# Performance work log

Hardware: AMD Instinct MI355X
Metric: run time of the kernel (lower is better)

## Reference

```python
import jax, jax.numpy as jnp
import numpy as np

DIM = 384
HEADS = 8


def setup_inputs() -> dict:
    key = jax.random.key(0)
    ks = jax.random.split(key, 8)
    d = DIM
    return {
        "x": jax.random.normal(ks[0], (4, d, 128, 128), jnp.float32),
        "message": jax.random.normal(ks[1], (4, d, 128, 128), jnp.float32),
        "temperature": jnp.ones((HEADS, 1, 1), jnp.float32),
        "qkv_w": jax.random.normal(ks[2], (3 * d, d), jnp.float32) * 0.02,   # 1x1 conv weight
        "dw_w": jax.random.normal(ks[3], (3 * d, 1, 3, 3), jnp.float32) * 0.02,  # depthwise 3x3
        "proj_w": jax.random.normal(ks[4], (d, d), jnp.float32) * 0.02,     # project_out 1x1
        "lin_w": jax.random.normal(ks[5], (d, 2 * d), jnp.float32) * 0.02,  # nn.Linear weight [out,in]
        "lin_b": jnp.zeros((d,), jnp.float32),
    }


def _qkv_branch(t, qkv_w, dw_w):
    # 1x1 conv (pointwise) then depthwise 3x3, groups = 3*dim
    y = jnp.einsum('oc,bchw->bohw', qkv_w, t)
    y = jax.lax.conv_general_dilated(
        y, dw_w, window_strides=(1, 1), padding='SAME',
        dimension_numbers=('NCHW', 'OIHW', 'NCHW'),
        feature_group_count=dw_w.shape[0])
    return jnp.split(y, 3, axis=1)  # q, k, v each [b, dim, h, w]


def _to_heads(t):
    b, c, h, w = t.shape
    return t.reshape(b, HEADS, c // HEADS, h * w)  # [b, head, c, n]


def _l2norm(t):
    # torch F.normalize(dim=-1, eps=1e-12)
    n = jnp.sqrt(jnp.sum(t * t, axis=-1, keepdims=True))
    return t / jnp.maximum(n, 1e-12)


def reference(x, message, temperature, qkv_w, dw_w, proj_w, lin_w, lin_b):
    b, c, h, w = x.shape
    q, k, v = (_to_heads(t) for t in _qkv_branch(x, qkv_w, dw_w))
    q_m, k_m, v_m = (_to_heads(t) for t in _qkv_branch(message, qkv_w, dw_w))

    k_c = jnp.concatenate([k, k_m], axis=2)   # [b, head, 2c, n]
    v_c = jnp.concatenate([v, v_m], axis=2)

    q = _l2norm(q)
    k_c = _l2norm(k_c)
    q_m = _l2norm(q_m)

    # channel attention: [b, head, c, 2c]
    attn1 = jax.nn.softmax(jnp.einsum('bhcn,bhdn->bhcd', q, k_c) * temperature, axis=-1)
    attn2 = jax.nn.softmax(jnp.einsum('bhcn,bhdn->bhcd', q_m, k_c) * temperature, axis=-1)

    out1 = jnp.einsum('bhcd,bhdn->bhcn', attn1, v_c)  # [b, head, c, n]
    out2 = jnp.einsum('bhcd,bhdn->bhcn', attn2, v_c)

    # 'b head c (h w) -> b (h w) (head c)'
    out1 = out1.transpose(0, 3, 1, 2).reshape(b, h * w, c)
    out2 = out2.transpose(0, 3, 1, 2).reshape(b, h * w, c)

    cat = jnp.concatenate([out1, out2], axis=2)  # [b, n, 2c]
    out = cat @ lin_w.T + lin_b                  # [b, n, c]

    # 'b (h w) c -> b c h w'
    out = out.transpose(0, 2, 1).reshape(b, c, h, w)
    out = jnp.einsum('oc,bchw->bohw', proj_w, out)
    return out
```

## Files before the change

kernel.cpp:

```cpp
#include <hip/hip_runtime.h>

typedef unsigned short u16;
typedef unsigned int u32;

#define BATCH 4
#define CDIM 384
#define IMG 128
#define HW 16384
#define QKVC 1152
#define NHEADS 8
#define CHD 48
#define DD2 96
#define KFIN 768

typedef __attribute__((ext_vector_type(8))) short bf16x8;
typedef __attribute__((ext_vector_type(4))) float f32x4;

__device__ __forceinline__ u16 f2bf(float f){
  union { float f; u32 u; } v; v.f = f;
  u32 u = v.u;
  u32 r = (u + 0x7fffu + ((u >> 16) & 1u)) >> 16;
  return (u16)r;
}
__device__ __forceinline__ float bf2f(u16 h){
  union { u32 u; float f; } v; v.u = ((u32)h) << 16;
  return v.f;
}

#define OFF_QKVX  ((size_t)0)
#define OFF_QKVM  ((size_t)150994944)
#define OFF_T     ((size_t)301989888)
#define OFF_SSQ   ((size_t)339738624)
#define OFF_S     ((size_t)339775488)
#define OFF_ATTN  ((size_t)340955136)
#define OFF_AFINB ((size_t)342134784)
#define OFF_W2    ((size_t)344494080)
#define OFF_B2    ((size_t)345673728)
#define OFF_WB    ((size_t)345675264)

typedef __attribute__((address_space(1))) const u32 gas_u32;
typedef __attribute__((address_space(3))) u32 las_u32;
__device__ __forceinline__ void gl_lds16(const u16* g, u16* l){
  __builtin_amdgcn_global_load_lds((gas_u32*)g, (las_u32*)l, 16, 0, 0);
}

__device__ __forceinline__ u16* t_row(u16* T0, u16* qkvm, int par, int ch){
  if (par == 0) return T0 + (size_t)ch * HW;
  int bq = ch / 384;
  int rr = ch - bq * 384;
  return qkvm + ((size_t)bq * QKVC + 2 * CDIM + rr) * HW;
}

__global__ void __launch_bounds__(256) k_w2(const float* __restrict__ proj,
                                            const float* __restrict__ lin,
                                            const float* __restrict__ linb,
                                            const float* __restrict__ qkvw,
                                            float* __restrict__ W2,
                                            float* __restrict__ b2,
                                            u16* __restrict__ Wb){
  int idx = blockIdx.x * 256 + threadIdx.x;
  if (idx < CDIM * KFIN){
    int o = idx / KFIN, d = idx % KFIN;
    float acc = 0.f;
    for (int c = 0; c < CDIM; c++)
      acc = fmaf(proj[o * CDIM + c], lin[c * KFIN + d], acc);
    W2[idx] = acc;
  }
  if (idx < CDIM){
    float acc = 0.f;
    for (int c = 0; c < CDIM; c++)
      acc = fmaf(proj[idx * CDIM + c], linb[c], acc);
    b2[idx] = acc;
  }
  if (idx < QKVC * CDIM) Wb[idx] = f2bf(qkvw[idx]);
}

__device__ __forceinline__ void loadrow(const u16* __restrict__ src, int r, int cg, float* o){
  if ((unsigned)r >= IMG){
    #pragma unroll
    for (int i = 0; i < 18; i++) o[i] = 0.f;
    return;
  }
  const u16* p = src + (size_t)r * IMG + cg * 16;
  uint4 v0 = *(const uint4*)p;
  uint4 v1 = *(const uint4*)(p + 8);
  u32 ww[8] = {v0.x, v0.y, v0.z, v0.w, v1.x, v1.y, v1.z, v1.w};
  #pragma unroll
  for (int i = 0; i < 8; i++){
    union { u32 u; float f; } lo, hi;
    lo.u = ww[i] << 16;
    hi.u = ww[i] & 0xffff0000u;
    o[1 + 2 * i] = lo.f;
    o[2 + 2 * i] = hi.f;
  }
  o[0]  = (cg > 0) ? bf2f(p[-1]) : 0.f;
  o[17] = (cg < 7) ? bf2f(p[16]) : 0.f;
}

__global__ void __launch_bounds__(256) k_stage(
    int t, int npw, int ndw,
    const u16* __restrict__ Wb, u16* __restrict__ Bt,
    u16* __restrict__ T0, u16* __restrict__ qkvx, u16* __restrict__ qkvm,
    const float* __restrict__ x, const float* __restrict__ msg,
    const float* __restrict__ dww, float* __restrict__ ssq){
  __shared__ __align__(16) u16 smem[16384];
  int bid = blockIdx.x;
  int tid = threadIdx.x;

  if (bid < npw){
    int z = t - 1, par = z & 1;
    const u16* B = Bt + (size_t)z * HW * CDIM;
    u16* As = smem;
    u16* Bs = smem + 8192;
    int swz = (bid & 7) * 144 + (bid >> 3);
    int bx = swz % 9, by = swz / 9;
    int m0 = bx * 128, n0 = by * 128;
    int w = tid >> 6, lane = tid & 63;
    int wy = w >> 1, wx = w & 1;
    int lm = lane & 15, q = lane >> 4;

    int srow = w * 16 + (lane >> 2);
    int scol = (lane & 3) * 8;
    const u16* ga = Wb + (size_t)(m0 + srow) * CDIM + scol;
    const u16* gb = B + (size_t)(n0 + srow) * CDIM + scol;
    u16* la = As + srow * 32 + scol;
    u16* lb = Bs + srow * 32 + scol;

    f32x4 acc[4][4];
    #pragma unroll
    for (int i = 0; i < 4; i++)
      #pragma unroll
      for (int j = 0; j < 4; j++) acc[i][j] = (f32x4){0.f,0.f,0.f,0.f};

#define PW_STAGE(buf, k0) do{ \
      gl_lds16(ga + (k0),             la + (buf) * 4096); \
      gl_lds16(ga + 64*CDIM + (k0),   la + (buf) * 4096 + 2048); \
      gl_lds16(gb + (k0),             lb + (buf) * 4096); \
      gl_lds16(gb + 64*CDIM + (k0),   lb + (buf) * 4096 + 2048); \
    }while(0)

    PW_STAGE(0, 0);
    __syncthreads();
    int cur = 0;
    for (int kt = 0; kt < 12; kt++){
      if (kt < 11) PW_STAGE(cur ^ 1, (kt + 1) * 32);
      bf16x8 af[4], bfr[4];
      #pragma unroll
      for (int i = 0; i < 4; i++)
        af[i] = *(const bf16x8*)&As[cur * 4096 + (wy * 64 + i * 16 + lm) * 32 + q * 8];
      #pragma unroll
      for (int j = 0; j < 4; j++)
        bfr[j] = *(const bf16x8*)&Bs[cur * 4096 + (wx * 64 + j * 16 + lm) * 32 + q * 8];
      #pragma unroll
      for (int i = 0; i < 4; i++)
        #pragma unroll
        for (int j = 0; j < 4; j++)
          acc[i][j] = __builtin_amdgcn_mfma_f32_16x16x32_bf16(af[i], bfr[j], acc[i][j], 0, 0, 0);
      __syncthreads();
      cur ^= 1;
    }
#undef PW_STAGE
    #pragma unroll
    for (int i = 0; i < 4; i++){
      #pragma unroll
      for (int r = 0; r < 4; r++){
        int row = m0 + wy * 64 + i * 16 + q * 4 + r;
        u16* cp = t_row(T0, qkvm, par, row) + n0 + wx * 64 + lm;
        #pragma unroll
        for (int j = 0; j < 4; j++)
          cp[j * 16] = f2bf(acc[i][j][r]);
      }
    }

  } else if (bid < npw + ndw){
    int ch = bid - npw;
    int z = t - 2, par = z & 1;
    const u16* src = t_row(T0, qkvm, par, ch);
    u16* dst;
    if (ch < 2 * CDIM){
      u16* qd = ((z >> 2) ? qkvm : qkvx) + (size_t)(z & 3) * QKVC * HW;
      dst = qd + (size_t)ch * HW;
    } else {
      dst = Bt + (size_t)z * HW * CDIM + (size_t)(ch - 2 * CDIM) * HW;
    }
    float w[9];
    #pragma unroll
    for (int t9 = 0; t9 < 9; t9++) w[t9] = dww[ch * 9 + t9];
    int rg = tid >> 3, cg = tid & 7;
    int r0 = rg * 4;
    float ra[18], rb[18], rc[18];
    loadrow(src, r0 - 1, cg, ra);
    loadrow(src, r0,     cg, rb);
    float ss = 0.f;
    #pragma unroll
    for (int rr = 0; rr < 4; rr++){
      int r = r0 + rr;
      loadrow(src, r + 1, cg, rc);
      u32 pk[8];
      #pragma unroll
      for (int xx = 0; xx < 16; xx++){
        float a2 = w[0] * ra[xx];
        a2 = fmaf(w[1], ra[xx + 1], a2);
        a2 = fmaf(w[2], ra[xx + 2], a2);
        a2 = fmaf(w[3], rb[xx],     a2);
        a2 = fmaf(w[4], rb[xx + 1], a2);
        a2 = fmaf(w[5], rb[xx + 2], a2);
        a2 = fmaf(w[6], rc[xx],     a2);
        a2 = fmaf(w[7], rc[xx + 1], a2);
        a2 = fmaf(w[8], rc[xx + 2], a2);
        ss = fmaf(a2, a2, ss);
        u16 hv = f2bf(a2);
        if (xx & 1) pk[xx >> 1] |= (u32)hv << 16;
        else        pk[xx >> 1]  = (u32)hv;
      }
      *(uint4*)(dst + (size_t)r * IMG + cg * 16)     = *(uint4*)&pk[0];
      *(uint4*)(dst + (size_t)r * IMG + cg * 16 + 8) = *(uint4*)&pk[4];
      #pragma unroll
      for (int ii = 0; ii < 18; ii++){ ra[ii] = rb[ii]; rb[ii] = rc[ii]; }
    }
    if (ch < 2 * CDIM){
      float* red = (float*)smem;
      red[tid] = ss;
      __syncthreads();
      for (int s = 128; s > 0; s >>= 1){
        if (tid < s) red[tid] += red[tid + s];
        __syncthreads();
      }
      if (tid == 0) ssq[(size_t)z * QKVC + ch] = red[0];
    }

  } else {
    int cb = bid - npw - ndw;
    int z = t;
    const float* src = (z < 4 ? x : msg) + (size_t)(z & 3) * CDIM * HW;
    u16* dstz = Bt + (size_t)z * HW * CDIM;
    int n0 = (cb & 127) * 128;
    int c0 = (cb >> 7) * 64;
    u16 (*tile)[130] = (u16(*)[130])smem;
    #pragma unroll
    for (int i = 0; i < 8; i++){
      int c = (tid >> 5) + i * 8;
      int nq = tid & 31;
      float4 v = *(const float4*)(src + (size_t)(c0 + c) * HW + n0 + nq * 4);
      u32 p0 = (u32)f2bf(v.x) | ((u32)f2bf(v.y) << 16);
      u32 p1 = (u32)f2bf(v.z) | ((u32)f2bf(v.w) << 16);
      *(u32*)&tile[c][nq * 4]     = p0;
      *(u32*)&tile[c][nq * 4 + 2] = p1;
    }
    __syncthreads();
    #pragma unroll
    for (int u = 0; u < 2; u++){
      int idx = tid + u * 256;
      int n = idx >> 2, j = idx & 3;
      u32 pk[8];
      #pragma unroll
      for (int p = 0; p < 8; p++)
        pk[p] = (u32)tile[j * 16 + 2 * p][n] | ((u32)tile[j * 16 + 2 * p + 1][n] << 16);
      u16* dp = dstz + (size_t)(n0 + n) * CDIM + c0 + j * 16;
      *(uint4*)dp       = *(uint4*)&pk[0];
      *(uint4*)(dp + 8) = *(uint4*)&pk[4];
    }
  }
}

#define LCHUNK 1024
__global__ void __launch_bounds__(256) k_tail(u16* __restrict__ qkvx,
                                              u16* __restrict__ qkvm,
                                              float* __restrict__ S,
                                              const u16* __restrict__ Bt){
  __shared__ u16 tile[48][136];
  int bid = blockIdx.x;
  int tid = threadIdx.x;

  if (bid < 512){
    int nc = bid & 15;
    int bh = bid >> 4;
    int b = bh & 3, h = bh >> 2;
    int w = tid >> 6, lane = tid & 63;
    int wy = w >> 1, wx = w & 1;
    int lm = lane & 15, quad = lane >> 4;

    const u16* ap[3]; const u16* bp[3];
    #pragma unroll
    for (int i = 0; i < 3; i++){
      int g = wy * 48 + i * 16 + lm;
      int c = (g < 48) ? g : g - 48;
      ap[i] = ((g < 48) ? qkvx : qkvm) + ((size_t)b * QKVC + h * CHD + c) * HW;
      int d = wx * 48 + i * 16 + lm;
      int cc = (d < 48) ? d : d - 48;
      bp[i] = ((d < 48) ? qkvx : qkvm) + ((size_t)b * QKVC + CDIM + h * CHD + cc) * HW;
    }
    f32x4 acc[3][3];
    #pragma unroll
    for (int i = 0; i < 3; i++)
      #pragma unroll
      for (int j = 0; j < 3; j++) acc[i][j] = (f32x4){0.f,0.f,0.f,0.f};

    int nbeg = nc * LCHUNK + quad * 8;
    int nend = nc * LCHUNK + LCHUNK;
    for (int n = nbeg; n < nend; n += 32){
      bf16x8 af[3], bfr[3];
      #pragma unroll
      for (int i = 0; i < 3; i++) af[i]  = *(const bf16x8*)(ap[i] + n);
      #pragma unroll
      for (int j = 0; j < 3; j++) bfr[j] = *(const bf16x8*)(bp[j] + n);
      #pragma unroll
      for (int i = 0; i < 3; i++)
        #pragma unroll
        for (int j = 0; j < 3; j++)
          acc[i][j] = __builtin_amdgcn_mfma_f32_16x16x32_bf16(af[i], bfr[j], acc[i][j], 0, 0, 0);
    }
    #pragma unroll
    for (int i = 0; i < 3; i++){
      #pragma unroll
      for (int r = 0; r < 4; r++){
        int g = wy * 48 + i * 16 + quad * 4 + r;
        int iq = (g >= 48) ? 1 : 0;
        int c = iq ? g - 48 : g;
        float* Sp = S + (((size_t)(iq * BATCH + b) * NHEADS + h) * CHD + c) * DD2;
        #pragma unroll
        for (int j = 0; j < 3; j++)
          atomicAdd(&Sp[wx * 48 + j * 16 + lm], acc[i][j][r]);
      }
    }
  } else {
    int v = bid - 512;
    int nb = v & 127;
    int h = (v >> 7) & 7;
    int z = v >> 10;
    int inp = z >> 2, b = z & 3;
    const u16* vcn = Bt + (size_t)z * HW * CDIM;
    int n0 = nb * 128;
    u16* vt = (h < 4 ? qkvx : qkvm) + ((size_t)b * QKVC + 2 * CDIM) * HW;
    int dbase = (h & 3) * 96 + inp * 48;
    #pragma unroll
    for (int j = 0; j < 3; j++){
      int i = tid + j * 256;
      int row = i >> 4, c8 = i & 15;
      uint4 vv = *(const uint4*)(vcn + (size_t)(h * 48 + row) * HW + n0 + c8 * 8);
      *(uint4*)&tile[row][c8 * 8] = vv;
    }
    __syncthreads();
    int n = tid >> 1, half = tid & 1;
    u16* dstp = vt + (size_t)(n0 + n) * CDIM + dbase + half * 24;
    #pragma unroll
    for (int u = 0; u < 3; u++){
      u32 pk[4];
      #pragma unroll
      for (int p = 0; p < 4; p++){
        int c = half * 24 + u * 8 + p * 2;
        pk[p] = (u32)tile[c][n] | ((u32)tile[c + 1][n] << 16);
      }
      *(uint4*)(dstp + u * 8) = *(uint4*)pk;
    }
  }
}

__global__ void __launch_bounds__(128) k_softmax(const float* __restrict__ S,
                                                 const float* __restrict__ ssq,
                                                 const float* __restrict__ temp,
                                                 float* __restrict__ attn){
  int row = blockIdx.x;
  int c = row % CHD;
  int h = (row / CHD) % NHEADS;
  int b = (row / (CHD * NHEADS)) % BATCH;
  int iq = row / (CHD * NHEADS * BATCH);
  int tid = threadIdx.x;
  __shared__ float sh[128];
  const float* Sp = S + (size_t)row * DD2;
  float ssq_q = ssq[(iq * BATCH + b) * QKVC + h * CHD + c];
  float nq = fmaxf(sqrtf(ssq_q), 1e-12f);
  float tmp = temp[h];
  float logit = -1e30f;
  int d = tid;
  if (d < DD2){
    float ssq_k = ssq[((d < CHD ? 0 : 1) * BATCH + b) * QKVC + CDIM + h * CHD + (d % CHD)];
    float nk = fmaxf(sqrtf(ssq_k), 1e-12f);
    logit = Sp[d] * tmp / (nq * nk);
  }
  sh[tid] = logit; __syncthreads();
  for (int s = 64; s > 0; s >>= 1){
    if (tid < s) sh[tid] = fmaxf(sh[tid], sh[tid + s]);
    __syncthreads();
  }
  float mx = sh[0]; __syncthreads();
  float e = (d < DD2) ? expf(logit - mx) : 0.f;
  sh[tid] = e; __syncthreads();
  for (int s = 64; s > 0; s >>= 1){
    if (tid < s) sh[tid] += sh[tid + s];
    __syncthreads();
  }
  float sum = sh[0];
  if (d < DD2) attn[(size_t)row * DD2 + d] = e / sum;
}

__global__ void __launch_bounds__(128) k_mmat(const float* __restrict__ attn,
                                              const float* __restrict__ W2,
                                              u16* __restrict__ AfinB){
  int oz = blockIdx.x;
  int h = blockIdx.y;
  int b = blockIdx.z;
  __shared__ float a1[CHD * DD2];
  __shared__ float a2[CHD * DD2];
  int tid = threadIdx.x;
  const float* A1 = attn + ((size_t)(0 * BATCH + b) * NHEADS + h) * CHD * DD2;
  const float* A2 = attn + ((size_t)(1 * BATCH + b) * NHEADS + h) * CHD * DD2;
  for (int i = tid; i < CHD * DD2; i += 128){ a1[i] = A1[i]; a2[i] = A2[i]; }
  __syncthreads();
  int e = tid;
  if (e < DD2){
    for (int oo = 0; oo < 8; oo++){
      int o = oz * 8 + oo;
      float acc = 0.f;
      #pragma unroll 4
      for (int cc = 0; cc < CHD; cc++){
        acc = fmaf(W2[o * KFIN + h * CHD + cc],        a1[cc * DD2 + e], acc);
        acc = fmaf(W2[o * KFIN + CDIM + h * CHD + cc], a2[cc * DD2 + e], acc);
      }
      AfinB[((size_t)b * CDIM + o) * KFIN + h * DD2 + e] = f2bf(acc);
    }
  }
}

__global__ void __launch_bounds__(256) k_fin(const u16* __restrict__ AfB,
                                             const u16* __restrict__ qkvx,
                                             const u16* __restrict__ qkvm,
                                             const float* __restrict__ b2,
                                             float* __restrict__ out){
  __shared__ __align__(16) u16 As[2 * 4096];
  __shared__ __align__(16) u16 Bs[2 * 4096];
  int orig = blockIdx.x;
  int swz = (orig & 7) * 192 + (orig >> 3);
  int m = swz % 3;
  int rest = swz / 3;
  int n0 = (rest & 127) * 128;
  int bz = rest >> 7;
  int m0 = m * 128;
  int tid = threadIdx.x;
  int w = tid >> 6, lane = tid & 63;
  int wy = w >> 1, wx = w & 1;
  int lm = lane & 15, q = lane >> 4;

  int srow = w * 16 + (lane >> 2);
  int scol = (lane & 3) * 8;
  const u16* A = AfB + (size_t)bz * CDIM * KFIN;
  const u16* ga  = A + (size_t)(m0 + srow) * KFIN + scol;
  const u16* gb0 = qkvx + ((size_t)bz * QKVC + 2 * CDIM) * HW + (size_t)(n0 + srow) * CDIM + scol;
  const u16* gb1 = qkvm + ((size_t)bz * QKVC + 2 * CDIM) * HW + (size_t)(n0 + srow) * CDIM + scol;
  u16* la = As + srow * 32 + scol;
  u16* lb = Bs + srow * 32 + scol;

  f32x4 acc[4][4];
  #pragma unroll
  for (int i = 0; i < 4; i++)
    #pragma unroll
    for (int j = 0; j < 4; j++) acc[i][j] = (f32x4){0.f,0.f,0.f,0.f};

#define FIN_STAGE(buf, t) do{ \
    int hp_ = (t) >= 12; \
    int k0_ = ((t) - hp_ * 12) * 32; \
    const u16* gb_ = hp_ ? gb1 : gb0; \
    gl_lds16(ga + hp_ * CDIM + k0_,            la + (buf) * 4096); \
    gl_lds16(ga + hp_ * CDIM + k0_ + 64*KFIN,  la + (buf) * 4096 + 2048); \
    gl_lds16(gb_ + k0_,                        lb + (buf) * 4096); \
    gl_lds16(gb_ + k0_ + 64*CDIM,              lb + (buf) * 4096 + 2048); \
  }while(0)

  FIN_STAGE(0, 0);
  __syncthreads();
  int cur = 0;
  for (int t = 0; t < 24; t++){
    if (t < 23) FIN_STAGE(cur ^ 1, t + 1);
    bf16x8 af[4], bfr[4];
    #pragma unroll
    for (int i = 0; i < 4; i++)
      af[i] = *(const bf16x8*)&As[cur * 4096 + (wy * 64 + i * 16 + lm) * 32 + q * 8];
    #pragma unroll
    for (int j = 0; j < 4; j++)
      bfr[j] = *(const bf16x8*)&Bs[cur * 4096 + (wx * 64 + j * 16 + lm) * 32 + q * 8];
    #pragma unroll
    for (int i = 0; i < 4; i++)
      #pragma unroll
      for (int j = 0; j < 4; j++)
        acc[i][j] = __builtin_amdgcn_mfma_f32_16x16x32_bf16(af[i], bfr[j], acc[i][j], 0, 0, 0);
    __syncthreads();
    cur ^= 1;
  }
#undef FIN_STAGE
  #pragma unroll
  for (int i = 0; i < 4; i++){
    #pragma unroll
    for (int r = 0; r < 4; r++){
      int row = m0 + wy * 64 + i * 16 + q * 4 + r;
      float bv = b2[row];
      float* cp = out + (size_t)bz * CDIM * HW + (size_t)row * HW + n0 + wx * 64 + lm;
      #pragma unroll
      for (int j = 0; j < 4; j++)
        cp[j * 16] = acc[i][j][r] + bv;
    }
  }
}

extern "C" void kernel_launch(void* const* d_in, const int* in_sizes, int n_in,
                              void* d_out, int out_size, void* d_ws, size_t ws_size,
                              hipStream_t stream){
  const float* x      = (const float*)d_in[0];
  const float* msg    = (const float*)d_in[1];
  const float* temp   = (const float*)d_in[2];
  const float* qkv_w  = (const float*)d_in[3];
  const float* dw_w   = (const float*)d_in[4];
  const float* proj_w = (const float*)d_in[5];
  const float* lin_w  = (const float*)d_in[6];
  const float* lin_b  = (const float*)d_in[7];
  float* out = (float*)d_out;

  char* ws = (char*)d_ws;
  u16*   qkvx  = (u16*)(ws + OFF_QKVX);
  u16*   qkvm  = (u16*)(ws + OFF_QKVM);
  u16*   T0    = (u16*)(ws + OFF_T);
  float* ssq   = (float*)(ws + OFF_SSQ);
  float* S     = (float*)(ws + OFF_S);
  float* attn  = (float*)(ws + OFF_ATTN);
  u16*   AfinB = (u16*)(ws + OFF_AFINB);
  float* W2    = (float*)(ws + OFF_W2);
  float* b2    = (float*)(ws + OFF_B2);
  u16*   Wb    = (u16*)(ws + OFF_WB);

  u16* Bt = (u16*)d_out;

  hipMemsetAsync(ws + OFF_S, 0, (OFF_ATTN - OFF_S), stream);

  k_w2<<<dim3((QKVC * CDIM + 255) / 256), dim3(256), 0, stream>>>(
      proj_w, lin_w, lin_b, qkv_w, W2, b2, Wb);

  for (int t = 0; t < 10; t++){
    int npw  = (t >= 1 && t <= 8) ? 1152 : 0;
    int ndw  = (t >= 2) ? 1152 : 0;
    int ncvt = (t < 8) ? 768 : 0;
    k_stage<<<dim3(npw + ndw + ncvt), dim3(256), 0, stream>>>(
        t, npw, ndw, Wb, Bt, T0, qkvx, qkvm, x, msg, dw_w, ssq);
  }

  k_tail<<<dim3(512 + 8192), dim3(256), 0, stream>>>(qkvx, qkvm, S, Bt);
  k_softmax<<<dim3(2 * BATCH * NHEADS * CHD), dim3(128), 0, stream>>>(S, ssq, temp, attn);
  k_mmat<<<dim3(CDIM / 8, NHEADS, BATCH), dim3(128), 0, stream>>>(attn, W2, AfinB);
  k_fin<<<dim3(3 * (HW / 128) * BATCH), dim3(256), 0, stream>>>(
      AfinB, qkvx, qkvm, b2, out);
}
```

Measured before the change: 843.3 us.

## Fold attention logits and V transpose into the staged pipeline kernel

Removes the separate k_tail kernel. Its QK-logit accumulation and V transpose blocks now run as extra roles inside the per-step k_stage launches, with one added step. V transposes are spread across stages as each batch's data becomes ready, and logits for a batch are computed once its q/k are done. This lets small, latency-bound work overlap with the pointwise and depthwise phases instead of running serially at the end. The V-transpose store pattern is also reorganised into 6 parts of 8 channels per row. The main risk is in the stage and readiness indexing (for example, logits for batch b computed at step t=b+7), which must match when each batch's data is actually written.

```diff
diff --git a/kernel.cpp b/kernel.cpp
--- a/kernel.cpp
+++ b/kernel.cpp
@@ -97,12 +97,14 @@
   o[17] = (cg < 7) ? bf2f(p[16]) : 0.f;
 }
 
+#define LCHUNK 1024
 __global__ void __launch_bounds__(256) k_stage(
-    int t, int npw, int ndw,
+    int t, int npw, int nlog, int ndw, int ncvt,
     const u16* __restrict__ Wb, u16* __restrict__ Bt,
     u16* __restrict__ T0, u16* __restrict__ qkvx, u16* __restrict__ qkvm,
     const float* __restrict__ x, const float* __restrict__ msg,
-    const float* __restrict__ dww, float* __restrict__ ssq){
+    const float* __restrict__ dww, float* __restrict__ ssq,
+    float* __restrict__ S){
   __shared__ __align__(16) u16 smem[16384];
   int bid = blockIdx.x;
   int tid = threadIdx.x;
@@ -172,8 +174,61 @@
       }
     }
 
-  } else if (bid < npw + ndw){
-    int ch = bid - npw;
+  } else if (bid < npw + nlog){
+    int idx = bid - npw;
+    int b = t - 7;
+    int nc = idx & 15;
+    int h = idx >> 4;
+    int w = tid >> 6, lane = tid & 63;
+    int wy = w >> 1, wx = w & 1;
+    int lm = lane & 15, quad = lane >> 4;
+
+    const u16* ap[3]; const u16* bp[3];
+    #pragma unroll
+    for (int i = 0; i < 3; i++){
+      int g = wy * 48 + i * 16 + lm;
+      int c = (g < 48) ? g : g - 48;
+      ap[i] = ((g < 48) ? qkvx : qkvm) + ((size_t)b * QKVC + h * CHD + c) * HW;
+      int d = wx * 48 + i * 16 + lm;
+      int cc = (d < 48) ? d : d - 48;
+      bp[i] = ((d < 48) ? qkvx : qkvm) + ((size_t)b * QKVC + CDIM + h * CHD + cc) * HW;
+    }
+    f32x4 acc[3][3];
+    #pragma unroll
+    for (int i = 0; i < 3; i++)
+      #pragma unroll
+      for (int j = 0; j < 3; j++) acc[i][j] = (f32x4){0.f,0.f,0.f,0.f};
+
+    int nbeg = nc * LCHUNK + quad * 8;
+    int nend = nc * LCHUNK + LCHUNK;
+    for (int n = nbeg; n < nend; n += 32){
+      bf16x8 af[3], bfr[3];
+      #pragma unroll
+      for (int i = 0; i < 3; i++) af[i]  = *(const bf16x8*)(ap[i] + n);
+      #pragma unroll
+      for (int j = 0; j < 3; j++) bfr[j] = *(const bf16x8*)(bp[j] + n);
+      #pragma unroll
+      for (int i = 0; i < 3; i++)
+        #pragma unroll
+        for (int j = 0; j < 3; j++)
+          acc[i][j] = __builtin_amdgcn_mfma_f32_16x16x32_bf16(af[i], bfr[j], acc[i][j], 0, 0, 0);
+    }
+    #pragma unroll
+    for (int i = 0; i < 3; i++){
+      #pragma unroll
+      for (int r = 0; r < 4; r++){
+        int g = wy * 48 + i * 16 + quad * 4 + r;
+        int iq = (g >= 48) ? 1 : 0;
+        int c = iq ? g - 48 : g;
+        float* Sp = S + (((size_t)(iq * BATCH + b) * NHEADS + h) * CHD + c) * DD2;
+        #pragma unroll
+        for (int j = 0; j < 3; j++)
+          atomicAdd(&Sp[wx * 48 + j * 16 + lm], acc[i][j][r]);
+      }
+    }
+
+  } else if (bid < npw + nlog + ndw){
+    int ch = bid - npw - nlog;
     int z = t - 2, par = z & 1;
     const u16* src = t_row(T0, qkvm, par, ch);
     u16* dst;
@@ -229,8 +284,8 @@
       if (tid == 0) ssq[(size_t)z * QKVC + ch] = red[0];
     }
 
-  } else {
-    int cb = bid - npw - ndw;
+  } else if (bid < npw + nlog + ndw + ncvt){
+    int cb = bid - npw - nlog - ndw;
     int z = t;
     const float* src = (z < 4 ? x : msg) + (size_t)(z & 3) * CDIM * HW;
     u16* dstz = Bt + (size_t)z * HW * CDIM;
@@ -260,79 +315,18 @@
       *(uint4*)dp       = *(uint4*)&pk[0];
       *(uint4*)(dp + 8) = *(uint4*)&pk[4];
     }
-  }
-}
-
-#define LCHUNK 1024
-__global__ void __launch_bounds__(256) k_tail(u16* __restrict__ qkvx,
-                                              u16* __restrict__ qkvm,
-                                              float* __restrict__ S,
-                                              const u16* __restrict__ Bt){
-  __shared__ u16 tile[48][136];
-  int bid = blockIdx.x;
-  int tid = threadIdx.x;
-
-  if (bid < 512){
-    int nc = bid & 15;
-    int bh = bid >> 4;
-    int b = bh & 3, h = bh >> 2;
-    int w = tid >> 6, lane = tid & 63;
-    int wy = w >> 1, wx = w & 1;
-    int lm = lane & 15, quad = lane >> 4;
-
-    const u16* ap[3]; const u16* bp[3];
-    #pragma unroll
-    for (int i = 0; i < 3; i++){
-      int g = wy * 48 + i * 16 + lm;
-      int c = (g < 48) ? g : g - 48;
-      ap[i] = ((g < 48) ? qkvx : qkvm) + ((size_t)b * QKVC + h * CHD + c) * HW;
-      int d = wx * 48 + i * 16 + lm;
-      int cc = (d < 48) ? d : d - 48;
-      bp[i] = ((d < 48) ? qkvx : qkvm) + ((size_t)b * QKVC + CDIM + h * CHD + cc) * HW;
-    }
-    f32x4 acc[3][3];
-    #pragma unroll
-    for (int i = 0; i < 3; i++)
-      #pragma unroll
-      for (int j = 0; j < 3; j++) acc[i][j] = (f32x4){0.f,0.f,0.f,0.f};
-
-    int nbeg = nc * LCHUNK + quad * 8;
-    int nend = nc * LCHUNK + LCHUNK;
-    for (int n = nbeg; n < nend; n += 32){
-      bf16x8 af[3], bfr[3];
-      #pragma unroll
-      for (int i = 0; i < 3; i++) af[i]  = *(const bf16x8*)(ap[i] + n);
-      #pragma unroll
-      for (int j = 0; j < 3; j++) bfr[j] = *(const bf16x8*)(bp[j] + n);
-      #pragma unroll
-      for (int i = 0; i < 3; i++)
-        #pragma unroll
-        for (int j = 0; j < 3; j++)
-          acc[i][j] = __builtin_amdgcn_mfma_f32_16x16x32_bf16(af[i], bfr[j], acc[i][j], 0, 0, 0);
-    }
-    #pragma unroll
-    for (int i = 0; i < 3; i++){
-      #pragma unroll
-      for (int r = 0; r < 4; r++){
-        int g = wy * 48 + i * 16 + quad * 4 + r;
-        int iq = (g >= 48) ? 1 : 0;
-        int c = iq ? g - 48 : g;
-        float* Sp = S + (((size_t)(iq * BATCH + b) * NHEADS + h) * CHD + c) * DD2;
-        #pragma unroll
-        for (int j = 0; j < 3; j++)
-          atomicAdd(&Sp[wx * 48 + j * 16 + lm], acc[i][j][r]);
-      }
-    }
+
   } else {
-    int v = bid - 512;
-    int nb = v & 127;
-    int h = (v >> 7) & 7;
-    int z = v >> 10;
+    int v = bid - npw - nlog - ndw - ncvt;
+    int z, h, nb;
+    if (v < 512){ z = t - 3; h = v >> 7; nb = v & 127; }
+    else { int u = v - 512; z = u >> 9; h = 4 + ((u >> 7) & 3); nb = u & 127; }
     int inp = z >> 2, b = z & 3;
     const u16* vcn = Bt + (size_t)z * HW * CDIM;
     int n0 = nb * 128;
     u16* vt = (h < 4 ? qkvx : qkvm) + ((size_t)b * QKVC + 2 * CDIM) * HW;
     int dbase = (h & 3) * 96 + inp * 48;
+    u16 (*tile)[136] = (u16(*)[136])smem;
     #pragma unroll
     for (int j = 0; j < 3; j++){
       int i = tid + j * 256;
@@ -341,17 +335,17 @@
       *(uint4*)&tile[row][c8 * 8] = vv;
     }
     __syncthreads();
-    int n = tid >> 1, half = tid & 1;
-    u16* dstp = vt + (size_t)(n0 + n) * CDIM + dbase + half * 24;
-    #pragma unroll
-    for (int u = 0; u < 3; u++){
+    #pragma unroll
+    for (int pass = 0; pass < 3; pass++){
+      int idx = tid + pass * 256;
+      int n = idx / 6, part = idx - n * 6;
       u32 pk[4];
       #pragma unroll
       for (int p = 0; p < 4; p++){
-        int c = half * 24 + u * 8 + p * 2;
+        int c = part * 8 + p * 2;
         pk[p] = (u32)tile[c][n] | ((u32)tile[c + 1][n] << 16);
       }
-      *(uint4*)(dstp + u * 8) = *(uint4*)pk;
+      *(uint4*)(vt + (size_t)(n0 + n) * CDIM + dbase + part * 8) = *(uint4*)pk;
     }
   }
 }
@@ -533,15 +527,16 @@
   k_w2<<<dim3((QKVC * CDIM + 255) / 256), dim3(256), 0, stream>>>(
       proj_w, lin_w, lin_b, qkv_w, W2, b2, Wb);
 
-  for (int t = 0; t < 10; t++){
+  for (int t = 0; t < 11; t++){
     int npw  = (t >= 1 && t <= 8) ? 1152 : 0;
-    int ndw  = (t >= 2) ? 1152 : 0;
-    int ncvt = (t < 8) ? 768 : 0;
-    k_stage<<<dim3(npw + ndw + ncvt), dim3(256), 0, stream>>>(
-        t, npw, ndw, Wb, Bt, T0, qkvx, qkvm, x, msg, dw_w, ssq);
-  }
-
-  k_tail<<<dim3(512 + 8192), dim3(256), 0, stream>>>(qkvx, qkvm, S, Bt);
+    int ndw  = (t >= 2 && t <= 9) ? 1152 : 0;
+    int ncvt = (t <= 7) ? 768 : 0;
+    int nlog = (t >= 7) ? 128 : 0;
+    int nvt  = (t >= 3) ? ((t == 10) ? 4608 : 512) : 0;
+    k_stage<<<dim3(npw + nlog + ndw + ncvt + nvt), dim3(256), 0, stream>>>(
+        t, npw, nlog, ndw, ncvt, Wb, Bt, T0, qkvx, qkvm, x, msg, dw_w, ssq, S);
+  }
+
   k_softmax<<<dim3(2 * BATCH * NHEADS * CHD), dim3(128), 0, stream>>>(S, ssq, temp, attn);
   k_mmat<<<dim3(CDIM / 8, NHEADS, BATCH), dim3(128), 0, stream>>>(attn, W2, AfinB);
   k_fin<<<dim3(3 * (HW / 128) * BATCH), dim3(256), 0, stream>>>(
```

After: 881.4 us. +4.5%, slower.

## Split fused staged pipeline into separate convert, pointwise GEMM and depthwise kernels

Applied to the files above, without the earlier changes.

Replaces the software-pipelined k_stage launches, which overlapped GEMM, depthwise and conversion work across batches, with a single bulk conversion kernel followed by per-batch alternating pointwise-GEMM and depthwise kernels sharing one T buffer. This removes the branchy mixed-role kernel and the ping-pong buffer aliasing into qkvm, but loses cross-stage overlap and adds more launches. The tail kernel's S-GEMM loop is also unrolled by two to issue more loads before the MFMAs, and the V-transpose store is remapped so each thread writes 8-element parts across 768 slots.

```diff
diff --git a/kernel.cpp b/kernel.cpp
--- a/kernel.cpp
+++ b/kernel.cpp
@@ -42,13 +42,6 @@
 typedef __attribute__((address_space(3))) u32 las_u32;
 __device__ __forceinline__ void gl_lds16(const u16* g, u16* l){
   __builtin_amdgcn_global_load_lds((gas_u32*)g, (las_u32*)l, 16, 0, 0);
-}
-
-__device__ __forceinline__ u16* t_row(u16* T0, u16* qkvm, int par, int ch){
-  if (par == 0) return T0 + (size_t)ch * HW;
-  int bq = ch / 384;
-  int rr = ch - bq * 384;
-  return qkvm + ((size_t)bq * QKVC + 2 * CDIM + rr) * HW;
 }
 
 __global__ void __launch_bounds__(256) k_w2(const float* __restrict__ proj,
@@ -75,6 +68,111 @@
   if (idx < QKVC * CDIM) Wb[idx] = f2bf(qkvw[idx]);
 }
 
+__global__ void __launch_bounds__(256) k_cvt(const float* __restrict__ x,
+                                             const float* __restrict__ msg,
+                                             u16* __restrict__ Bt){
+  int bid = blockIdx.x;
+  int z = bid / 768;
+  int cb = bid - z * 768;
+  const float* src = (z < 4 ? x : msg) + (size_t)(z & 3) * CDIM * HW;
+  u16* dstz = Bt + (size_t)z * HW * CDIM;
+  int n0 = (cb & 127) * 128;
+  int c0 = (cb >> 7) * 64;
+  __shared__ u16 tile[64][130];
+  int tid = threadIdx.x;
+  #pragma unroll
+  for (int i = 0; i < 8; i++){
+    int c = (tid >> 5) + i * 8;
+    int nq = tid & 31;
+    float4 v = *(const float4*)(src + (size_t)(c0 + c) * HW + n0 + nq * 4);
+    u32 p0 = (u32)f2bf(v.x) | ((u32)f2bf(v.y) << 16);
+    u32 p1 = (u32)f2bf(v.z) | ((u32)f2bf(v.w) << 16);
+    *(u32*)&tile[c][nq * 4]     = p0;
+    *(u32*)&tile[c][nq * 4 + 2] = p1;
+  }
+  __syncthreads();
+  #pragma unroll
+  for (int u = 0; u < 2; u++){
+    int idx = tid + u * 256;
+    int n = idx >> 2, j = idx & 3;
+    u32 pk[8];
+    #pragma unroll
+    for (int p = 0; p < 8; p++)
+      pk[p] = (u32)tile[j * 16 + 2 * p][n] | ((u32)tile[j * 16 + 2 * p + 1][n] << 16);
+    u16* dp = dstz + (size_t)(n0 + n) * CDIM + c0 + j * 16;
+    *(uint4*)dp       = *(uint4*)&pk[0];
+    *(uint4*)(dp + 8) = *(uint4*)&pk[4];
+  }
+}
+
+__global__ void __launch_bounds__(256) k_pw(const u16* __restrict__ A,
+                                            const u16* __restrict__ B,
+                                            u16* __restrict__ C){
+  __shared__ __align__(16) u16 As[2 * 4096];
+  __shared__ __align__(16) u16 Bs[2 * 4096];
+  int orig = blockIdx.x;
+  int swz = (orig & 7) * 144 + (orig >> 3);
+  int bx = swz % 9, by = swz / 9;
+  int m0 = bx * 128, n0 = by * 128;
+  int tid = threadIdx.x;
+  int w = tid >> 6, lane = tid & 63;
+  int wy = w >> 1, wx = w & 1;
+  int lm = lane & 15, q = lane >> 4;
+
+  int srow = w * 16 + (lane >> 2);
+  int scol = (lane & 3) * 8;
+  const u16* ga = A + (size_t)(m0 + srow) * CDIM + scol;
+  const u16* gb = B + (size_t)(n0 + srow) * CDIM + scol;
+  u16* la = As + srow * 32 + scol;
+  u16* lb = Bs + srow * 32 + scol;
+
+  f32x4 acc[4][4];
+  #pragma unroll
+  for (int i = 0; i < 4; i++)
+    #pragma unroll
+    for (int j = 0; j < 4; j++) acc[i][j] = (f32x4){0.f,0.f,0.f,0.f};
+
+#define PW_STAGE(buf, k0) do{ \
+    gl_lds16(ga + (k0),             la + (buf) * 4096); \
+    gl_lds16(ga + 64*CDIM + (k0),   la + (buf) * 4096 + 2048); \
+    gl_lds16(gb + (k0),             lb + (buf) * 4096); \
+    gl_lds16(gb + 64*CDIM + (k0),   lb + (buf) * 4096 + 2048); \
+  }while(0)
+
+  PW_STAGE(0, 0);
+  __syncthreads();
+  int cur = 0;
+  for (int t = 0; t < 12; t++){
+    if (t < 11) PW_STAGE(cur ^ 1, (t + 1) * 32);
+    bf16x8 af[4], bfr[4];
+    #pragma unroll
+    for (int i = 0; i < 4; i++)
+      af[i] = *(const bf16x8*)&As[cur * 4096 + (wy * 64 + i * 16 + lm) * 32 + q * 8];
+    #pragma unroll
+    for (int j = 0; j < 4; j++)
+      bfr[j] = *(const bf16x8*)&Bs[cur * 4096 + (wx * 64 + j * 16 + lm) * 32 + q * 8];
+    #pragma unroll
+    for (int i = 0; i < 4; i++)
+      #pragma unroll
+      for (int j = 0; j < 4; j++)
+        acc[i][j] = __builtin_amdgcn_mfma_f32_16x16x32_bf16(af[i], bfr[j], acc[i][j], 0, 0, 0);
+    __syncthreads();
+    cur ^= 1;
+  }
+#undef PW_STAGE
+  #pragma unroll
+  for (int i = 0; i < 4; i++){
+    #pragma unroll
+    for (int r = 0; r < 4; r++){
+      int row = m0 + wy * 64 + i * 16 + q * 4 + r;
+      u16* cp = C + (size_t)row * HW + n0 + wx * 64 + lm;
+      #pragma unroll
+      for (int j = 0; j < 4; j++)
+        cp[j * 16] = f2bf(acc[i][j][r]);
+    }
+  }
+}
+
 __device__ __forceinline__ void loadrow(const u16* __restrict__ src, int r, int cg, float* o){
   if ((unsigned)r >= IMG){
     #pragma unroll
@@ -97,169 +195,60 @@
   o[17] = (cg < 7) ? bf2f(p[16]) : 0.f;
 }
 
-__global__ void __launch_bounds__(256) k_stage(
-    int t, int npw, int ndw,
-    const u16* __restrict__ Wb, u16* __restrict__ Bt,
-    u16* __restrict__ T0, u16* __restrict__ qkvx, u16* __restrict__ qkvm,
-    const float* __restrict__ x, const float* __restrict__ msg,
-    const float* __restrict__ dww, float* __restrict__ ssq){
-  __shared__ __align__(16) u16 smem[16384];
-  int bid = blockIdx.x;
-  int tid = threadIdx.x;
-
-  if (bid < npw){
-    int z = t - 1, par = z & 1;
-    const u16* B = Bt + (size_t)z * HW * CDIM;
-    u16* As = smem;
-    u16* Bs = smem + 8192;
-    int swz = (bid & 7) * 144 + (bid >> 3);
-    int bx = swz % 9, by = swz / 9;
-    int m0 = bx * 128, n0 = by * 128;
-    int w = tid >> 6, lane = tid & 63;
-    int wy = w >> 1, wx = w & 1;
-    int lm = lane & 15, q = lane >> 4;
-
-    int srow = w * 16 + (lane >> 2);
-    int scol = (lane & 3) * 8;
-    const u16* ga = Wb + (size_t)(m0 + srow) * CDIM + scol;
-    const u16* gb = B + (size_t)(n0 + srow) * CDIM + scol;
-    u16* la = As + srow * 32 + scol;
-    u16* lb = Bs + srow * 32 + scol;
-
-    f32x4 acc[4][4];
-    #pragma unroll
-    for (int i = 0; i < 4; i++)
-      #pragma unroll
-      for (int j = 0; j < 4; j++) acc[i][j] = (f32x4){0.f,0.f,0.f,0.f};
-
-#define PW_STAGE(buf, k0) do{ \
-      gl_lds16(ga + (k0),             la + (buf) * 4096); \
-      gl_lds16(ga + 64*CDIM + (k0),   la + (buf) * 4096 + 2048); \
-      gl_lds16(gb + (k0),             lb + (buf) * 4096); \
-      gl_lds16(gb + 64*CDIM + (k0),   lb + (buf) * 4096 + 2048); \
-    }while(0)
-
-    PW_STAGE(0, 0);
+__global__ void __launch_bounds__(256) k_dw2(const u16* __restrict__ T,
+                                             const float* __restrict__ dw,
+                                             u16* __restrict__ qdst,
+                                             u16* __restrict__ vdst,
+                                             float* __restrict__ ssq){
+  int ch = blockIdx.x;
+  const u16* src = T + (size_t)ch * HW;
+  u16* dst = (ch < 2 * CDIM) ? qdst + (size_t)ch * HW
+                             : vdst + (size_t)(ch - 2 * CDIM) * HW;
+  float w[9];
+  #pragma unroll
+  for (int t = 0; t < 9; t++) w[t] = dw[ch * 9 + t];
+  int tid = threadIdx.x;
+  int rg = tid >> 3, cg = tid & 7;
+  int r0 = rg * 4;
+  float ra[18], rb[18], rc[18];
+  loadrow(src, r0 - 1, cg, ra);
+  loadrow(src, r0,     cg, rb);
+  float ss = 0.f;
+  #pragma unroll
+  for (int rr = 0; rr < 4; rr++){
+    int r = r0 + rr;
+    loadrow(src, r + 1, cg, rc);
+    u32 pk[8];
+    #pragma unroll
+    for (int xx = 0; xx < 16; xx++){
+      float a2 = w[0] * ra[xx];
+      a2 = fmaf(w[1], ra[xx + 1], a2);
+      a2 = fmaf(w[2], ra[xx + 2], a2);
+      a2 = fmaf(w[3], rb[xx],     a2);
+      a2 = fmaf(w[4], rb[xx + 1], a2);
+      a2 = fmaf(w[5], rb[xx + 2], a2);
+      a2 = fmaf(w[6], rc[xx],     a2);
+      a2 = fmaf(w[7], rc[xx + 1], a2);
+      a2 = fmaf(w[8], rc[xx + 2], a2);
+      ss = fmaf(a2, a2, ss);
+      u16 hv = f2bf(a2);
+      if (xx & 1) pk[xx >> 1] |= (u32)hv << 16;
+      else        pk[xx >> 1]  = (u32)hv;
+    }
+    *(uint4*)(dst + (size_t)r * IMG + cg * 16)     = *(uint4*)&pk[0];
+    *(uint4*)(dst + (size_t)r * IMG + cg * 16 + 8) = *(uint4*)&pk[4];
+    #pragma unroll
+    for (int ii = 0; ii < 18; ii++){ ra[ii] = rb[ii]; rb[ii] = rc[ii]; }
+  }
+  if (ch < 2 * CDIM){
+    __shared__ float red[256];
+    red[tid] = ss;
     __syncthreads();
-    int cur = 0;
-    for (int kt = 0; kt < 12; kt++){
-      if (kt < 11) PW_STAGE(cur ^ 1, (kt + 1) * 32);
-      bf16x8 af[4], bfr[4];
-      #pragma unroll
-      for (int i = 0; i < 4; i++)
-        af[i] = *(const bf16x8*)&As[cur * 4096 + (wy * 64 + i * 16 + lm) * 32 + q * 8];
-      #pragma unroll
-      for (int j = 0; j < 4; j++)
-        bfr[j] = *(const bf16x8*)&Bs[cur * 4096 + (wx * 64 + j * 16 + lm) * 32 + q * 8];
-      #pragma unroll
-      for (int i = 0; i < 4; i++)
-        #pragma unroll
-        for (int j = 0; j < 4; j++)
-          acc[i][j] = __builtin_amdgcn_mfma_f32_16x16x32_bf16(af[i], bfr[j], acc[i][j], 0, 0, 0);
+    for (int s = 128; s > 0; s >>= 1){
+      if (tid < s) red[tid] += red[tid + s];
       __syncthreads();
-      cur ^= 1;
-    }
-#undef PW_STAGE
-    #pragma unroll
-    for (int i = 0; i < 4; i++){
-      #pragma unroll
-      for (int r = 0; r < 4; r++){
-        int row = m0 + wy * 64 + i * 16 + q * 4 + r;
-        u16* cp = t_row(T0, qkvm, par, row) + n0 + wx * 64 + lm;
-        #pragma unroll
-        for (int j = 0; j < 4; j++)
-          cp[j * 16] = f2bf(acc[i][j][r]);
-      }
-    }
-
-  } else if (bid < npw + ndw){
-    int ch = bid - npw;
-    int z = t - 2, par = z & 1;
-    const u16* src = t_row(T0, qkvm, par, ch);
-    u16* dst;
-    if (ch < 2 * CDIM){
-      u16* qd = ((z >> 2) ? qkvm : qkvx) + (size_t)(z & 3) * QKVC * HW;
-      dst = qd + (size_t)ch * HW;
-    } else {
-      dst = Bt + (size_t)z * HW * CDIM + (size_t)(ch - 2 * CDIM) * HW;
-    }
-    float w[9];
-    #pragma unroll
-    for (int t9 = 0; t9 < 9; t9++) w[t9] = dww[ch * 9 + t9];
-    int rg = tid >> 3, cg = tid & 7;
-    int r0 = rg * 4;
-    float ra[18], rb[18], rc[18];
-    loadrow(src, r0 - 1, cg, ra);
-    loadrow(src, r0,     cg, rb);
-    float ss = 0.f;
-    #pragma unroll
-    for (int rr = 0; rr < 4; rr++){
-      int r = r0 + rr;
-      loadrow(src, r + 1, cg, rc);
-      u32 pk[8];
-      #pragma unroll
-      for (int xx = 0; xx < 16; xx++){
-        float a2 = w[0] * ra[xx];
-        a2 = fmaf(w[1], ra[xx + 1], a2);
-        a2 = fmaf(w[2], ra[xx + 2], a2);
-        a2 = fmaf(w[3], rb[xx],     a2);
-        a2 = fmaf(w[4], rb[xx + 1], a2);
-        a2 = fmaf(w[5], rb[xx + 2], a2);
-        a2 = fmaf(w[6], rc[xx],     a2);
-        a2 = fmaf(w[7], rc[xx + 1], a2);
-        a2 = fmaf(w[8], rc[xx + 2], a2);
-        ss = fmaf(a2, a2, ss);
-        u16 hv = f2bf(a2);
-        if (xx & 1) pk[xx >> 1] |= (u32)hv << 16;
-        else        pk[xx >> 1]  = (u32)hv;
-      }
-      *(uint4*)(dst + (size_t)r * IMG + cg * 16)     = *(uint4*)&pk[0];
-      *(uint4*)(dst + (size_t)r * IMG + cg * 16 + 8) = *(uint4*)&pk[4];
-      #pragma unroll
-      for (int ii = 0; ii < 18; ii++){ ra[ii] = rb[ii]; rb[ii] = rc[ii]; }
-    }
-    if (ch < 2 * CDIM){
-      float* red = (float*)smem;
-      red[tid] = ss;
-      __syncthreads();
-      for (int s = 128; s > 0; s >>= 1){
-        if (tid < s) red[tid] += red[tid + s];
-        __syncthreads();
-      }
-      if (tid == 0) ssq[(size_t)z * QKVC + ch] = red[0];
-    }
-
-  } else {
-    int cb = bid - npw - ndw;
-    int z = t;
-    const float* src = (z < 4 ? x : msg) + (size_t)(z & 3) * CDIM * HW;
-    u16* dstz = Bt + (size_t)z * HW * CDIM;
-    int n0 = (cb & 127) * 128;
-    int c0 = (cb >> 7) * 64;
-    u16 (*tile)[130] = (u16(*)[130])smem;
-    #pragma unroll
-    for (int i = 0; i < 8; i++){
-      int c = (tid >> 5) + i * 8;
-      int nq = tid & 31;
-      float4 v = *(const float4*)(src + (size_t)(c0 + c) * HW + n0 + nq * 4);
-      u32 p0 = (u32)f2bf(v.x) | ((u32)f2bf(v.y) << 16);
-      u32 p1 = (u32)f2bf(v.z) | ((u32)f2bf(v.w) << 16);
-      *(u32*)&tile[c][nq * 4]     = p0;
-      *(u32*)&tile[c][nq * 4 + 2] = p1;
-    }
-    __syncthreads();
-    #pragma unroll
-    for (int u = 0; u < 2; u++){
-      int idx = tid + u * 256;
-      int n = idx >> 2, j = idx & 3;
-      u32 pk[8];
-      #pragma unroll
-      for (int p = 0; p < 8; p++)
-        pk[p] = (u32)tile[j * 16 + 2 * p][n] | ((u32)tile[j * 16 + 2 * p + 1][n] << 16);
-      u16* dp = dstz + (size_t)(n0 + n) * CDIM + c0 + j * 16;
-      *(uint4*)dp       = *(uint4*)&pk[0];
-      *(uint4*)(dp + 8) = *(uint4*)&pk[4];
-    }
+    }
+    if (tid == 0) ssq[ch] = red[0];
   }
 }
 
@@ -298,17 +287,28 @@
 
     int nbeg = nc * LCHUNK + quad * 8;
     int nend = nc * LCHUNK + LCHUNK;
-    for (int n = nbeg; n < nend; n += 32){
-      bf16x8 af[3], bfr[3];
-      #pragma unroll
-      for (int i = 0; i < 3; i++) af[i]  = *(const bf16x8*)(ap[i] + n);
-      #pragma unroll
-      for (int j = 0; j < 3; j++) bfr[j] = *(const bf16x8*)(bp[j] + n);
+    for (int n = nbeg; n < nend; n += 64){
+      bf16x8 af0[3], bf0[3], af1[3], bf1[3];
+      #pragma unroll
+      for (int i = 0; i < 3; i++){
+        af0[i] = *(const bf16x8*)(ap[i] + n);
+        af1[i] = *(const bf16x8*)(ap[i] + n + 32);
+      }
+      #pragma unroll
+      for (int j = 0; j < 3; j++){
+        bf0[j] = *(const bf16x8*)(bp[j] + n);
+        bf1[j] = *(const bf16x8*)(bp[j] + n + 32);
+      }
       #pragma unroll
       for (int i = 0; i < 3; i++)
         #pragma unroll
         for (int j = 0; j < 3; j++)
-          acc[i][j] = __builtin_amdgcn_mfma_f32_16x16x32_bf16(af[i], bfr[j], acc[i][j], 0, 0, 0);
+          acc[i][j] = __builtin_amdgcn_mfma_f32_16x16x32_bf16(af0[i], bf0[j], acc[i][j], 0, 0, 0);
+      #pragma unroll
+      for (int i = 0; i < 3; i++)
+        #pragma unroll
+        for (int j = 0; j < 3; j++)
+          acc[i][j] = __builtin_amdgcn_mfma_f32_16x16x32_bf16(af1[i], bf1[j], acc[i][j], 0, 0, 0);
     }
     #pragma unroll
     for (int i = 0; i < 3; i++){
@@ -341,17 +341,17 @@
       *(uint4*)&tile[row][c8 * 8] = vv;
     }
     __syncthreads();
-    int n = tid >> 1, half = tid & 1;
-    u16* dstp = vt + (size_t)(n0 + n) * CDIM + dbase + half * 24;
-    #pragma unroll
-    for (int u = 0; u < 3; u++){
+    #pragma unroll
+    for (int pass = 0; pass < 3; pass++){
+      int idx = tid + pass * 256;
+      int n = idx / 6, part = idx - n * 6;
       u32 pk[4];
       #pragma unroll
       for (int p = 0; p < 4; p++){
-        int c = half * 24 + u * 8 + p * 2;
+        int c = part * 8 + p * 2;
         pk[p] = (u32)tile[c][n] | ((u32)tile[c + 1][n] << 16);
       }
-      *(uint4*)(dstp + u * 8) = *(uint4*)pk;
+      *(uint4*)(vt + (size_t)(n0 + n) * CDIM + dbase + part * 8) = *(uint4*)pk;
     }
   }
 }
@@ -517,7 +517,7 @@
   char* ws = (char*)d_ws;
   u16*   qkvx  = (u16*)(ws + OFF_QKVX);
   u16*   qkvm  = (u16*)(ws + OFF_QKVM);
-  u16*   T0    = (u16*)(ws + OFF_T);
+  u16*   T     = (u16*)(ws + OFF_T);
   float* ssq   = (float*)(ws + OFF_SSQ);
   float* S     = (float*)(ws + OFF_S);
   float* attn  = (float*)(ws + OFF_ATTN);
@@ -533,12 +533,15 @@
   k_w2<<<dim3((QKVC * CDIM + 255) / 256), dim3(256), 0, stream>>>(
       proj_w, lin_w, lin_b, qkv_w, W2, b2, Wb);
 
-  for (int t = 0; t < 10; t++){
-    int npw  = (t >= 1 && t <= 8) ? 1152 : 0;
-    int ndw  = (t >= 2) ? 1152 : 0;
-    int ncvt = (t < 8) ? 768 : 0;
-    k_stage<<<dim3(npw + ndw + ncvt), dim3(256), 0, stream>>>(
-        t, npw, ndw, Wb, Bt, T0, qkvx, qkvm, x, msg, dw_w, ssq);
+  k_cvt<<<dim3(8 * 768), dim3(256), 0, stream>>>(x, msg, Bt);
+
+  for (int z = 0; z < 8; z++){
+    int inp = z >> 2, bb = z & 3;
+    u16* qdst = (inp ? qkvm : qkvx) + (size_t)bb * QKVC * HW;
+    k_pw<<<dim3(QKVC / 128 * (HW / 128)), dim3(256), 0, stream>>>(
+        Wb, Bt + (size_t)z * HW * CDIM, T);
+    k_dw2<<<dim3(QKVC), dim3(256), 0, stream>>>(
+        T, dw_w, qdst, Bt + (size_t)z * HW * CDIM, ssq + (size_t)z * QKVC);
   }
 
   k_tail<<<dim3(512 + 8192), dim3(256), 0, stream>>>(qkvx, qkvm, S, Bt);
```

Result: slower. 911.0 us (+8.0%).
